# Kernel optimization log

Hardware: AMD Instinct MI355X
Metric: run time of the kernel (lower is better)

Reference implementation:

```python
import jax, jax.numpy as jnp
import numpy as np

N_NODES = 100000
N_EDGES = 3200000
D_IN = 256
D_HID = 97


def setup_inputs() -> dict:
    key = jax.random.key(0)
    k1, k2, k3, k4, k5, k6 = jax.random.split(key, 6)
    x = jax.random.normal(k1, (N_NODES, D_IN), dtype=jnp.float32)
    edge_index = jax.random.randint(k2, (2, N_EDGES), 0, N_NODES, dtype=jnp.int64)
    # GCNConv weights (stored as [in, out]) and biases
    W1 = jax.random.normal(k3, (D_IN, D_HID), dtype=jnp.float32) / np.sqrt(D_IN)
    b1 = jnp.zeros((D_HID,), dtype=jnp.float32)
    W2 = jax.random.normal(k4, (D_HID, D_HID), dtype=jnp.float32) / np.sqrt(D_HID)
    b2 = jnp.zeros((D_HID,), dtype=jnp.float32)
    return {"x": x, "edge_index": edge_index, "W1": W1, "b1": b1, "W2": W2, "b2": b2}


def reference(x, edge_index, W1, b1, W2, b2):
    # PyG GCNConv: add self-loops, symmetric degree normalization,
    # out[i] = sum_j norm_ij * (x[j] @ W) + b
    N = x.shape[0]
    self_idx = jnp.arange(N, dtype=edge_index.dtype)
    src = jnp.concatenate([edge_index[0], self_idx])  # source j
    dst = jnp.concatenate([edge_index[1], self_idx])  # target i
    deg = jax.ops.segment_sum(jnp.ones_like(dst, dtype=x.dtype), dst, num_segments=N)
    dinv = jnp.where(deg > 0, 1.0 / jnp.sqrt(deg), 0.0)
    norm = dinv[src] * dinv[dst]  # [E+N]

    def gcn(h, W, b):
        h = h @ W  # dense linear transform first (out_dim small)
        msg = h[src] * norm[:, None]  # gather + scale
        agg = jax.ops.segment_sum(msg, dst, num_segments=N)  # scatter-add
        return agg + b

    h = jax.nn.relu(gcn(x, W1, b1))
    out = gcn(h, W2, b2)
    return out
```

## Files before the change

kernel.cpp:

```cpp
#include <hip/hip_runtime.h>
#include <hip/hip_fp16.h>
#include <stdint.h>

#define D_IN 256
#define D_H  97
#define RST  96
#define NPB  512
#define NBMAX 256
#define CHUNK 4096

typedef _Float16 f16;
typedef f16   f16x8 __attribute__((ext_vector_type(8)));
typedef float f32x4 __attribute__((ext_vector_type(4)));

__device__ __forceinline__ int load_idx(const void* p, int is64, long long pos) {
  if (is64) return (int)(((const long long*)p)[pos]);
  return ((const int*)p)[pos];
}

__global__ void detect_kernel(const void* ei, long long E, int* flag) {
  const int* p32 = (const int*)ei;
  long long stride = E / 1024; if (stride < 1) stride = 1;
  int tid = threadIdx.x;
  int bad = 0;
  for (int s = 0; s < 4; ++s) {
    long long k = ((long long)tid * 4 + s) * stride;
    if (k < E) {
      if (p32[2 * k + 1] != 0) bad = 1;
    }
  }
  __shared__ int sh_bad;
  if (tid == 0) sh_bad = 0;
  __syncthreads();
  if (bad) atomicOr(&sh_bad, 1);
  __syncthreads();
  if (tid == 0) *flag = sh_bad ? 0 : 1;
}

__global__ __launch_bounds__(256) void bucket_scatter_direct(
    const void* ei, const int* __restrict__ flag, int* __restrict__ bcur,
    unsigned int* __restrict__ bsd, long long E, int nbuck, int cap) {
  __shared__ unsigned int packs[CHUNK];
  __shared__ unsigned char bkts[CHUNK];
  __shared__ int hist[NBMAX];
  __shared__ int gpos[NBMAX];
  __shared__ int cur[NBMAX];
  int tid = threadIdx.x;
  if (tid < NBMAX) { hist[tid] = 0; cur[tid] = 0; }
  __syncthreads();
  int f = *flag;
  long long base = (long long)blockIdx.x * CHUNK;
  int cnt = (int)((E - base < CHUNK) ? (E - base) : CHUNK);
  #pragma unroll 4
  for (int i = tid; i < cnt; i += 256) {
    long long e = base + i;
    int s = load_idx(ei, f, e);
    int d = load_idx(ei, f, E + e);
    int b = d >> 9;
    packs[i] = ((unsigned int)(d & (NPB - 1)) << 17) | (unsigned int)s;
    bkts[i] = (unsigned char)b;
    atomicAdd(&hist[b], 1);
  }
  __syncthreads();
  if (tid < nbuck) { int h = hist[tid]; if (h) gpos[tid] = atomicAdd(&bcur[tid], h); }
  __syncthreads();
  #pragma unroll 4
  for (int i = tid; i < cnt; i += 256) {
    int b = bkts[i];
    int r = atomicAdd(&cur[b], 1);
    int idx = gpos[b] + r;
    if (idx < cap) bsd[(size_t)b * cap + idx] = packs[i];
  }
}

__global__ void bucket_scan2(const int* __restrict__ bcur, int* __restrict__ bstart,
                             int* __restrict__ row_start, int N, int nbuck, int cap) {
  __shared__ int sh[256];
  int tid = threadIdx.x;
  int v = (tid < nbuck) ? min(bcur[tid], cap) : 0;
  sh[tid] = v;
  __syncthreads();
  for (int off = 1; off < 256; off <<= 1) {
    int a = (tid >= off) ? sh[tid - off] : 0;
    __syncthreads();
    sh[tid] += a;
    __syncthreads();
  }
  if (tid < nbuck) bstart[tid] = sh[tid] - v;
  if (tid == 255) { bstart[nbuck] = sh[255]; row_start[N] = sh[255]; }
}

__global__ __launch_bounds__(256) void bucket_finalize(
    const unsigned int* __restrict__ bsd, const int* __restrict__ bcur,
    const int* __restrict__ bstart,
    int* __restrict__ row_start, float* __restrict__ dinv,
    int* __restrict__ csr_src, int N, int cap) {
  __shared__ int h[NPB];
  __shared__ int rs[NPB];
  __shared__ int cur[NPB];
  __shared__ int wsum[4];
  int b = blockIdx.x, tid = threadIdx.x;
  int lane = tid & 63, wid = tid >> 6;
  h[2 * tid] = 0; h[2 * tid + 1] = 0;
  cur[2 * tid] = 0; cur[2 * tid + 1] = 0;
  __syncthreads();
  int d0 = b * cap;
  int cnt = min(bcur[b], cap);
  for (int i = tid; i < cnt; i += 256) atomicAdd(&h[bsd[d0 + i] >> 17], 1);
  __syncthreads();
  int a0 = h[2 * tid], a1 = h[2 * tid + 1];
  int tsum = a0 + a1;
  int incl = tsum;
  #pragma unroll
  for (int off = 1; off < 64; off <<= 1) {
    int n = __shfl_up(incl, off, 64);
    if (lane >= off) incl += n;
  }
  if (lane == 63) wsum[wid] = incl;
  __syncthreads();
  int woff = 0;
  for (int k = 0; k < wid; ++k) woff += wsum[k];
  int excl = woff + incl - tsum + bstart[b];
  rs[2 * tid] = excl;
  rs[2 * tid + 1] = excl + a0;
  int node0 = b * NPB;
  int n0 = node0 + 2 * tid, n1 = node0 + 2 * tid + 1;
  if (n0 < N) { row_start[n0] = excl;      dinv[n0] = rsqrtf((float)(a0 + 1)); }
  if (n1 < N) { row_start[n1] = excl + a0; dinv[n1] = rsqrtf((float)(a1 + 1)); }
  __syncthreads();
  for (int i = tid; i < cnt; i += 256) {
    unsigned int p = bsd[d0 + i];
    int r = p >> 17;
    int s = (int)(p & 0x1FFFFu);
    int rel = atomicAdd(&cur[r], 1);
    csr_src[rs[r] + rel] = s;
  }
}

__global__ void prep_kernel(const float* __restrict__ W1, const float* __restrict__ b1,
                            const float* __restrict__ W2, const float* __restrict__ b2,
                            f16* __restrict__ W1lin, f16* __restrict__ W2lin,
                            float* __restrict__ b1p, float* __restrict__ b2p) {
  int idx = blockIdx.x * blockDim.x + threadIdx.x;
  const int n1 = 8 * 7 * 512;
  const int n2 = 4 * 7 * 512;
  if (idx < n1) {
    int fid = idx >> 3, hh = idx & 7;
    int lane = fid & 63, fg = fid >> 6;
    int kb = fg / 7, cg = fg % 7;
    int c = cg * 16 + (lane & 15);
    int k = kb * 32 + (lane >> 4) * 8 + hh;
    W1lin[idx] = (f16)((c < D_H && k < 256) ? W1[k * D_H + c] : 0.f);
  } else if (idx < n1 + n2) {
    int j = idx - n1;
    int fid = j >> 3, hh = j & 7;
    int lane = fid & 63, fg = fid >> 6;
    int kb = fg / 7, cg = fg % 7;
    int c = cg * 16 + (lane & 15);
    int k = kb * 32 + (lane >> 4) * 8 + hh;
    W2lin[j] = (f16)((c < D_H && k < D_H) ? W2[k * D_H + c] : 0.f);
  } else if (idx < n1 + n2 + 128) {
    int c = idx - (n1 + n2);
    b1p[c] = (c < D_H) ? b1[c] : 0.0f;
  } else if (idx < n1 + n2 + 256) {
    int c = idx - (n1 + n2 + 128);
    b2p[c] = (c < D_H) ? b2[c] : 0.0f;
  }
}

template<int KI, bool IN_HALF>
__global__ __launch_bounds__(256) void mfma_gemm(
    const float* __restrict__ Af, const f16* __restrict__ Ah,
    const __half2* __restrict__ sideA,
    const f16* __restrict__ Wlin, const float* __restrict__ dinv,
    f16* __restrict__ C, __half2* __restrict__ sideC, int N) {
  int tid = threadIdx.x, wave = tid >> 6, lane = tid & 63;
  int row0 = blockIdx.x * 128;
  int m = lane & 15, q = lane >> 4;
  int kf = q * 8;
  int r0 = row0 + wave * 32 + m;
  int r1 = r0 + 16;
  int rr0 = (r0 < N) ? r0 : 0;
  int rr1 = (r1 < N) ? r1 : 0;
  const f16* wbase = Wlin + lane * 8;

  f16x8 a0[KI], a1[KI];
  #pragma unroll
  for (int kb = 0; kb < KI; ++kb) {
    if constexpr (!IN_HALF) {
      const float* p0 = &Af[(size_t)rr0 * 256 + kb * 32 + kf];
      const float* p1 = &Af[(size_t)rr1 * 256 + kb * 32 + kf];
      float4 u0 = *(const float4*)p0, u1 = *(const float4*)(p0 + 4);
      float4 w0 = *(const float4*)p1, w1 = *(const float4*)(p1 + 4);
      f16x8 t0, t1;
      t0[0] = (f16)u0.x; t0[1] = (f16)u0.y; t0[2] = (f16)u0.z; t0[3] = (f16)u0.w;
      t0[4] = (f16)u1.x; t0[5] = (f16)u1.y; t0[6] = (f16)u1.z; t0[7] = (f16)u1.w;
      t1[0] = (f16)w0.x; t1[1] = (f16)w0.y; t1[2] = (f16)w0.z; t1[3] = (f16)w0.w;
      t1[4] = (f16)w1.x; t1[5] = (f16)w1.y; t1[6] = (f16)w1.z; t1[7] = (f16)w1.w;
      a0[kb] = t0; a1[kb] = t1;
    } else {
      if (kb < KI - 1) {
        a0[kb] = *(const f16x8*)&Ah[(size_t)rr0 * RST + kb * 32 + kf];
        a1[kb] = *(const f16x8*)&Ah[(size_t)rr1 * RST + kb * 32 + kf];
      } else {
        f16x8 z0, z1;
        #pragma unroll
        for (int j = 0; j < 8; ++j) { z0[j] = (f16)0.f; z1[j] = (f16)0.f; }
        if (q == 0) {
          z0[0] = ((const f16*)sideA)[2 * rr0];
          z1[0] = ((const f16*)sideA)[2 * rr1];
        }
        a0[kb] = z0; a1[kb] = z1;
      }
    }
  }

  f32x4 acc[2][7];
  #pragma unroll
  for (int mg = 0; mg < 2; ++mg)
    #pragma unroll
    for (int cg = 0; cg < 7; ++cg)
      #pragma unroll
      for (int j = 0; j < 4; ++j) acc[mg][cg][j] = 0.f;

  #pragma unroll
  for (int kb = 0; kb < KI; ++kb) {
    #pragma unroll
    for (int cg = 0; cg < 7; ++cg) {
      f16x8 b = *(const f16x8*)&wbase[(kb * 7 + cg) * 512];
      acc[0][cg] = __builtin_amdgcn_mfma_f32_16x16x32_f16(a0[kb], b, acc[0][cg], 0, 0, 0);
      acc[1][cg] = __builtin_amdgcn_mfma_f32_16x16x32_f16(a1[kb], b, acc[1][cg], 0, 0, 0);
    }
  }

  int colb = m, rq = q * 4;
  #pragma unroll
  for (int mg = 0; mg < 2; ++mg) {
    #pragma unroll
    for (int j = 0; j < 4; ++j) {
      int r = row0 + wave * 32 + mg * 16 + rq + j;
      if (r >= N) continue;
      float dv = dinv[r];
      #pragma unroll
      for (int cg = 0; cg < 7; ++cg) {
        int c = cg * 16 + colb;
        float val = acc[mg][cg][j] * dv;
        if (c < 96)       C[(size_t)r * RST + c] = (f16)val;
        else if (c == 96) sideC[r] = __floats2half2_rn(val, 0.f);
      }
    }
  }
}

template<bool OUT_HALF, bool DO_RELU>
__global__ __launch_bounds__(256) void agg_kernel(
    const __half* __restrict__ t, const __half2* __restrict__ side,
    const int* __restrict__ csr_src, const int* __restrict__ row_start,
    const float* __restrict__ dinv, const float* __restrict__ bias,
    void* __restrict__ outp, __half2* __restrict__ side_out, int node_base, int N) {
  int lane = threadIdx.x & 63;
  int node = node_base + blockIdx.x * (blockDim.x >> 6) + (threadIdx.x >> 6);
  if (node >= N || lane >= 49) return;
  const char* gbase = (lane < 48) ? (const char*)t + lane * 4 : (const char*)side;
  unsigned gscale = (lane < 48) ? (unsigned)(RST * 2) : 4u;
  auto GATHER = [&](int j) -> float2 {
    return __half22float2(*(const __half2*)(gbase + (size_t)((unsigned)j * gscale)));
  };
  int s = row_start[node], epd = row_start[node + 1];
  float di = dinv[node];
  float2 v = GATHER(node);
  float ax = v.x, ay = v.y;
  int e = s;
  while ((e & 3) && e < epd) {
    float2 u = GATHER(csr_src[e]);
    ax += u.x; ay += u.y; ++e;
  }
  for (; e + 8 <= epd; e += 8) {
    int4 q0 = *(const int4*)(csr_src + e);
    int4 q1 = *(const int4*)(csr_src + e + 4);
    float2 u0 = GATHER(q0.x), u1 = GATHER(q0.y), u2 = GATHER(q0.z), u3 = GATHER(q0.w);
    float2 u4 = GATHER(q1.x), u5 = GATHER(q1.y), u6 = GATHER(q1.z), u7 = GATHER(q1.w);
    ax += ((u0.x + u1.x) + (u2.x + u3.x)) + ((u4.x + u5.x) + (u6.x + u7.x));
    ay += ((u0.y + u1.y) + (u2.y + u3.y)) + ((u4.y + u5.y) + (u6.y + u7.y));
  }
  if (e + 4 <= epd) {
    int4 q0 = *(const int4*)(csr_src + e);
    float2 u0 = GATHER(q0.x), u1 = GATHER(q0.y), u2 = GATHER(q0.z), u3 = GATHER(q0.w);
    ax += (u0.x + u1.x) + (u2.x + u3.x);
    ay += (u0.y + u1.y) + (u2.y + u3.y);
    e += 4;
  }
  for (; e < epd; ++e) {
    float2 u = GATHER(csr_src[e]);
    ax += u.x; ay += u.y;
  }
  int c0 = 2 * lane;
  ax = ax * di + bias[c0];
  ay = ay * di + bias[c0 + 1];
  if (DO_RELU) { ax = fmaxf(ax, 0.f); ay = fmaxf(ay, 0.f); }
  if (OUT_HALF) {
    if (lane < 48) ((__half2*)((__half*)outp + (size_t)node * RST))[lane] = __floats2half2_rn(ax, ay);
    else           side_out[node] = __floats2half2_rn(ax, 0.f);
  } else {
    float* o = (float*)outp + (size_t)node * D_H;
    if (lane < 48) { o[c0] = ax; o[c0 + 1] = ay; }
    else           o[96] = ax;
  }
}

extern "C" void kernel_launch(void* const* d_in, const int* in_sizes, int n_in,
                              void* d_out, int out_size, void* d_ws, size_t ws_size,
                              hipStream_t stream) {
  const float* x  = (const float*)d_in[0];
  const void*  ei = d_in[1];
  const float* W1 = (const float*)d_in[2];
  const float* b1 = (const float*)d_in[3];
  const float* W2 = (const float*)d_in[4];
  const float* b2 = (const float*)d_in[5];
  int N = in_sizes[0] / D_IN;
  long long E = (long long)in_sizes[1] / 2;
  int nbuck = (N + NPB - 1) / NPB;
  int cap = (int)(E / nbuck) + 8192;

  char* base = (char*)d_ws;
  size_t off = 0;
  auto alloc = [&](size_t bytes) -> void* {
    void* p = base + off;
    off = (off + bytes + 255) & ~(size_t)255;
    return p;
  };
  int*    flag      = (int*)alloc(4);
  float*  dinv      = (float*)alloc((size_t)N * 4);
  int*    row_start = (int*)alloc((size_t)(N + 1) * 4);
  int*    bcur      = (int*)alloc((size_t)(nbuck + 1) * 4);
  int*    bstart    = (int*)alloc((size_t)(nbuck + 1) * 4);
  int*    csr_src   = (int*)alloc((size_t)E * 4);
  unsigned int* bsd = (unsigned int*)alloc((size_t)nbuck * cap * 4);
  f16*    W1lin     = (f16*)alloc((size_t)8 * 7 * 512 * 2);
  f16*    W2lin     = (f16*)alloc((size_t)4 * 7 * 512 * 2);
  float*  b1p       = (float*)alloc(128 * 4);
  float*  b2p       = (float*)alloc(128 * 4);
  f16*    t1        = (f16*)alloc((size_t)N * RST * 2 + 256);
  __half2* sideT    = (__half2*)alloc((size_t)N * 4 + 256);
  f16*    h1        = (f16*)alloc((size_t)N * RST * 2 + 256);
  __half2* sideH    = (__half2*)alloc((size_t)N * 4 + 256);

  hipMemsetAsync(bcur, 0, (size_t)(nbuck + 1) * 4, stream);
  detect_kernel<<<1, 256, 0, stream>>>(ei, E, flag);
  bucket_scatter_direct<<<(int)((E + CHUNK - 1) / CHUNK), 256, 0, stream>>>(
      ei, flag, bcur, bsd, E, nbuck, cap);
  bucket_scan2<<<1, 256, 0, stream>>>(bcur, bstart, row_start, N, nbuck, cap);
  bucket_finalize<<<nbuck, 256, 0, stream>>>(bsd, bcur, bstart, row_start, dinv, csr_src, N, cap);
  prep_kernel<<<(8 * 7 * 512 + 4 * 7 * 512 + 256 + 255) / 256, 256, 0, stream>>>(
      W1, b1, W2, b2, W1lin, W2lin, b1p, b2p);

  int gGemm = (N + 127) / 128;
  int half = N / 2;
  int gA0 = (half + 3) / 4;
  int gA1 = (N - half + 3) / 4;

  mfma_gemm<8, false><<<gGemm, 256, 0, stream>>>(
      x, nullptr, nullptr, W1lin, dinv, t1, sideT, N);
  agg_kernel<true, true><<<gA0, 256, 0, stream>>>(
      (const __half*)t1, sideT, csr_src, row_start, dinv, b1p, h1, sideH, 0, N);
  agg_kernel<true, true><<<gA1, 256, 0, stream>>>(
      (const __half*)t1, sideT, csr_src, row_start, dinv, b1p, h1, sideH, half, N);
  mfma_gemm<4, true><<<gGemm, 256, 0, stream>>>(
      nullptr, h1, sideH, W2lin, dinv, t1, sideT, N);
  agg_kernel<false, false><<<gA0, 256, 0, stream>>>(
      (const __half*)t1, sideT, csr_src, row_start, dinv, b2p, d_out, nullptr, 0, N);
  agg_kernel<false, false><<<gA1, 256, 0, stream>>>(
      (const __half*)t1, sideT, csr_src, row_start, dinv, b2p, d_out, nullptr, half, N);
}
```

Baseline: 374.2 us.

## Fuse second-layer GEMM into first aggregation and fold bucket scan into finalize

Layer 1's aggregation now multiplies each node's ReLU output by W2 from shared memory, so the second MFMA GEMM and the h1 round trip through global memory go away. The bucket prefix scan is recomputed inside every bucket_finalize block, and the bcur memset moves into detect_kernel, which removes two launches. The risk is that each 512-thread agg block must first copy the full ~19KB W2 into LDS, and per-node scalar GEMV work is added to a gather-bound kernel. The split agg launches are also merged into one.

New measurement: 396.5 us. 6.0% more time.

```diff
diff --git a/kernel.cpp b/kernel.cpp
--- a/kernel.cpp
+++ b/kernel.cpp
@@ -10,6 +10,7 @@
 #define CHUNK 4096
 
 typedef _Float16 f16;
+typedef f16   f16x2 __attribute__((ext_vector_type(2)));
 typedef f16   f16x8 __attribute__((ext_vector_type(8)));
 typedef float f32x4 __attribute__((ext_vector_type(4)));
 
@@ -18,10 +19,12 @@
   return ((const int*)p)[pos];
 }
 
-__global__ void detect_kernel(const void* ei, long long E, int* flag) {
+__global__ void detect_kernel(const void* ei, long long E, int* flag,
+                              int* __restrict__ bcur, int nbuck) {
   const int* p32 = (const int*)ei;
   long long stride = E / 1024; if (stride < 1) stride = 1;
   int tid = threadIdx.x;
+  for (int i = tid; i <= nbuck; i += 256) bcur[i] = 0;
   int bad = 0;
   for (int s = 0; s < 4; ++s) {
     long long k = ((long long)tid * 4 + s) * stride;
@@ -73,39 +76,32 @@
   }
 }
 
-__global__ void bucket_scan2(const int* __restrict__ bcur, int* __restrict__ bstart,
-                             int* __restrict__ row_start, int N, int nbuck, int cap) {
-  __shared__ int sh[256];
-  int tid = threadIdx.x;
-  int v = (tid < nbuck) ? min(bcur[tid], cap) : 0;
-  sh[tid] = v;
-  __syncthreads();
-  for (int off = 1; off < 256; off <<= 1) {
-    int a = (tid >= off) ? sh[tid - off] : 0;
-    __syncthreads();
-    sh[tid] += a;
-    __syncthreads();
-  }
-  if (tid < nbuck) bstart[tid] = sh[tid] - v;
-  if (tid == 255) { bstart[nbuck] = sh[255]; row_start[N] = sh[255]; }
-}
-
 __global__ __launch_bounds__(256) void bucket_finalize(
     const unsigned int* __restrict__ bsd, const int* __restrict__ bcur,
-    const int* __restrict__ bstart,
     int* __restrict__ row_start, float* __restrict__ dinv,
-    int* __restrict__ csr_src, int N, int cap) {
+    int* __restrict__ csr_src, int N, int cap, int nbuck) {
+  __shared__ int sc[256];
   __shared__ int h[NPB];
   __shared__ int rs[NPB];
   __shared__ int cur[NPB];
   __shared__ int wsum[4];
   int b = blockIdx.x, tid = threadIdx.x;
   int lane = tid & 63, wid = tid >> 6;
+  int v = (tid < nbuck) ? min(bcur[tid], cap) : 0;
+  sc[tid] = v;
   h[2 * tid] = 0; h[2 * tid + 1] = 0;
   cur[2 * tid] = 0; cur[2 * tid + 1] = 0;
   __syncthreads();
+  for (int o = 1; o < 256; o <<= 1) {
+    int a = (tid >= o) ? sc[tid - o] : 0;
+    __syncthreads();
+    sc[tid] += a;
+    __syncthreads();
+  }
+  int cnt = min(bcur[b], cap);
+  int base = sc[b] - cnt;
+  if (b == 0 && tid == 0) row_start[N] = sc[255];
   int d0 = b * cap;
-  int cnt = min(bcur[b], cap);
   for (int i = tid; i < cnt; i += 256) atomicAdd(&h[bsd[d0 + i] >> 17], 1);
   __syncthreads();
   int a0 = h[2 * tid], a1 = h[2 * tid + 1];
@@ -120,7 +116,7 @@
   __syncthreads();
   int woff = 0;
   for (int k = 0; k < wid; ++k) woff += wsum[k];
-  int excl = woff + incl - tsum + bstart[b];
+  int excl = woff + incl - tsum + base;
   rs[2 * tid] = excl;
   rs[2 * tid + 1] = excl + a0;
   int node0 = b * NPB;
@@ -139,11 +135,11 @@
 
 __global__ void prep_kernel(const float* __restrict__ W1, const float* __restrict__ b1,
                             const float* __restrict__ W2, const float* __restrict__ b2,
-                            f16* __restrict__ W1lin, f16* __restrict__ W2lin,
+                            f16* __restrict__ W1lin, f16* __restrict__ W2g,
                             float* __restrict__ b1p, float* __restrict__ b2p) {
   int idx = blockIdx.x * blockDim.x + threadIdx.x;
   const int n1 = 8 * 7 * 512;
-  const int n2 = 4 * 7 * 512;
+  const int n2 = 98 * 98;
   if (idx < n1) {
     int fid = idx >> 3, hh = idx & 7;
     int lane = fid & 63, fg = fid >> 6;
@@ -152,13 +148,8 @@
     int k = kb * 32 + (lane >> 4) * 8 + hh;
     W1lin[idx] = (f16)((c < D_H && k < 256) ? W1[k * D_H + c] : 0.f);
   } else if (idx < n1 + n2) {
-    int j = idx - n1;
-    int fid = j >> 3, hh = j & 7;
-    int lane = fid & 63, fg = fid >> 6;
-    int kb = fg / 7, cg = fg % 7;
-    int c = cg * 16 + (lane & 15);
-    int k = kb * 32 + (lane >> 4) * 8 + hh;
-    W2lin[j] = (f16)((c < D_H && k < D_H) ? W2[k * D_H + c] : 0.f);
+    int j = idx - n1; int k = j / 98, c = j % 98;
+    W2g[j] = (f16)((k < D_H && c < D_H) ? W2[k * D_H + c] : 0.f);
   } else if (idx < n1 + n2 + 128) {
     int c = idx - (n1 + n2);
     b1p[c] = (c < D_H) ? b1[c] : 0.0f;
@@ -168,12 +159,11 @@
   }
 }
 
-template<int KI, bool IN_HALF>
-__global__ __launch_bounds__(256) void mfma_gemm(
-    const float* __restrict__ Af, const f16* __restrict__ Ah,
-    const __half2* __restrict__ sideA,
-    const f16* __restrict__ Wlin, const float* __restrict__ dinv,
+__global__ __launch_bounds__(256) void mfma_gemm1(
+    const float* __restrict__ Af, const f16* __restrict__ Wlin,
+    const float* __restrict__ dinv,
     f16* __restrict__ C, __half2* __restrict__ sideC, int N) {
+  const int KI = 8;
   int tid = threadIdx.x, wave = tid >> 6, lane = tid & 63;
   int row0 = blockIdx.x * 128;
   int m = lane & 15, q = lane >> 4;
@@ -187,32 +177,16 @@
   f16x8 a0[KI], a1[KI];
   #pragma unroll
   for (int kb = 0; kb < KI; ++kb) {
-    if constexpr (!IN_HALF) {
-      const float* p0 = &Af[(size_t)rr0 * 256 + kb * 32 + kf];
-      const float* p1 = &Af[(size_t)rr1 * 256 + kb * 32 + kf];
-      float4 u0 = *(const float4*)p0, u1 = *(const float4*)(p0 + 4);
-      float4 w0 = *(const float4*)p1, w1 = *(const float4*)(p1 + 4);
-      f16x8 t0, t1;
-      t0[0] = (f16)u0.x; t0[1] = (f16)u0.y; t0[2] = (f16)u0.z; t0[3] = (f16)u0.w;
-      t0[4] = (f16)u1.x; t0[5] = (f16)u1.y; t0[6] = (f16)u1.z; t0[7] = (f16)u1.w;
-      t1[0] = (f16)w0.x; t1[1] = (f16)w0.y; t1[2] = (f16)w0.z; t1[3] = (f16)w0.w;
-      t1[4] = (f16)w1.x; t1[5] = (f16)w1.y; t1[6] = (f16)w1.z; t1[7] = (f16)w1.w;
-      a0[kb] = t0; a1[kb] = t1;
-    } else {
-      if (kb < KI - 1) {
-        a0[kb] = *(const f16x8*)&Ah[(size_t)rr0 * RST + kb * 32 + kf];
-        a1[kb] = *(const f16x8*)&Ah[(size_t)rr1 * RST + kb * 32 + kf];
-      } else {
-        f16x8 z0, z1;
-        #pragma unroll
-        for (int j = 0; j < 8; ++j) { z0[j] = (f16)0.f; z1[j] = (f16)0.f; }
-        if (q == 0) {
-          z0[0] = ((const f16*)sideA)[2 * rr0];
-          z1[0] = ((const f16*)sideA)[2 * rr1];
-        }
-        a0[kb] = z0; a1[kb] = z1;
-      }
-    }
+    const float* p0 = &Af[(size_t)rr0 * 256 + kb * 32 + kf];
+    const float* p1 = &Af[(size_t)rr1 * 256 + kb * 32 + kf];
+    float4 u0 = *(const float4*)p0, u1 = *(const float4*)(p0 + 4);
+    float4 w0 = *(const float4*)p1, w1 = *(const float4*)(p1 + 4);
+    f16x8 t0, t1;
+    t0[0] = (f16)u0.x; t0[1] = (f16)u0.y; t0[2] = (f16)u0.z; t0[3] = (f16)u0.w;
+    t0[4] = (f16)u1.x; t0[5] = (f16)u1.y; t0[6] = (f16)u1.z; t0[7] = (f16)u1.w;
+    t1[0] = (f16)w0.x; t1[1] = (f16)w0.y; t1[2] = (f16)w0.z; t1[3] = (f16)w0.w;
+    t1[4] = (f16)w1.x; t1[5] = (f16)w1.y; t1[6] = (f16)w1.z; t1[7] = (f16)w1.w;
+    a0[kb] = t0; a1[kb] = t1;
   }
 
   f32x4 acc[2][7];
@@ -252,25 +226,31 @@
   }
 }
 
-template<bool OUT_HALF, bool DO_RELU>
-__global__ __launch_bounds__(256) void agg_kernel(
+__global__ __launch_bounds__(512) void agg_gemv(
     const __half* __restrict__ t, const __half2* __restrict__ side,
     const int* __restrict__ csr_src, const int* __restrict__ row_start,
-    const float* __restrict__ dinv, const float* __restrict__ bias,
-    void* __restrict__ outp, __half2* __restrict__ side_out, int node_base, int N) {
-  int lane = threadIdx.x & 63;
-  int node = node_base + blockIdx.x * (blockDim.x >> 6) + (threadIdx.x >> 6);
+    const float* __restrict__ dinv, const float* __restrict__ b1p,
+    const f16* __restrict__ W2g,
+    f16* __restrict__ t2, __half2* __restrict__ side2, int N) {
+  __shared__ f16 W2s[98 * 98];
+  __shared__ float hbuf[8][98];
+  int tid = threadIdx.x;
+  for (int i = tid; i < 98 * 98 / 2; i += 512)
+    ((f16x2*)W2s)[i] = ((const f16x2*)W2g)[i];
+  __syncthreads();
+  int wave = tid >> 6, lane = tid & 63;
+  int node = blockIdx.x * 8 + wave;
   if (node >= N || lane >= 49) return;
+
   const char* gbase = (lane < 48) ? (const char*)t + lane * 4 : (const char*)side;
   unsigned gscale = (lane < 48) ? (unsigned)(RST * 2) : 4u;
   auto GATHER = [&](int j) -> float2 {
     return __half22float2(*(const __half2*)(gbase + (size_t)((unsigned)j * gscale)));
   };
-  int s = row_start[node], epd = row_start[node + 1];
+  int e = row_start[node], epd = row_start[node + 1];
   float di = dinv[node];
   float2 v = GATHER(node);
   float ax = v.x, ay = v.y;
-  int e = s;
   while ((e & 3) && e < epd) {
     float2 u = GATHER(csr_src[e]);
     ax += u.x; ay += u.y; ++e;
@@ -295,17 +275,81 @@
     ax += u.x; ay += u.y;
   }
   int c0 = 2 * lane;
+  ax = fmaxf(ax * di + b1p[c0], 0.f);
+  ay = fmaxf(ay * di + b1p[c0 + 1], 0.f);
+  hbuf[wave][c0] = ax;
+  if (c0 + 1 < 98) hbuf[wave][c0 + 1] = ay;
+
+  float s0 = 0.f, s1 = 0.f;
+  const float* hl = hbuf[wave];
+  #pragma unroll 4
+  for (int k = 0; k < 96; k += 2) {
+    float h0 = hl[k], h1 = hl[k + 1];
+    f16x2 w0 = *(const f16x2*)&W2s[k * 98 + c0];
+    f16x2 w1 = *(const f16x2*)&W2s[(k + 1) * 98 + c0];
+    s0 += h0 * (float)w0[0] + h1 * (float)w1[0];
+    s1 += h0 * (float)w0[1] + h1 * (float)w1[1];
+  }
+  {
+    float h96 = hl[96];
+    f16x2 w96 = *(const f16x2*)&W2s[96 * 98 + c0];
+    s0 += h96 * (float)w96[0];
+    s1 += h96 * (float)w96[1];
+  }
+  s0 *= di; s1 *= di;
+  if (lane < 48) {
+    *(__half2*)(&t2[(size_t)node * RST + c0]) = __floats2half2_rn(s0, s1);
+  } else {
+    side2[node] = __floats2half2_rn(s0, 0.f);
+  }
+}
+
+__global__ __launch_bounds__(256) void agg_out(
+    const __half* __restrict__ t, const __half2* __restrict__ side,
+    const int* __restrict__ csr_src, const int* __restrict__ row_start,
+    const float* __restrict__ dinv, const float* __restrict__ bias,
+    float* __restrict__ outp, int N) {
+  int lane = threadIdx.x & 63;
+  int node = blockIdx.x * (blockDim.x >> 6) + (threadIdx.x >> 6);
+  if (node >= N || lane >= 49) return;
+  const char* gbase = (lane < 48) ? (const char*)t + lane * 4 : (const char*)side;
+  unsigned gscale = (lane < 48) ? (unsigned)(RST * 2) : 4u;
+  auto GATHER = [&](int j) -> float2 {
+    return __half22float2(*(const __half2*)(gbase + (size_t)((unsigned)j * gscale)));
+  };
+  int e = row_start[node], epd = row_start[node + 1];
+  float di = dinv[node];
+  float2 v = GATHER(node);
+  float ax = v.x, ay = v.y;
+  while ((e & 3) && e < epd) {
+    float2 u = GATHER(csr_src[e]);
+    ax += u.x; ay += u.y; ++e;
+  }
+  for (; e + 8 <= epd; e += 8) {
+    int4 q0 = *(const int4*)(csr_src + e);
+    int4 q1 = *(const int4*)(csr_src + e + 4);
+    float2 u0 = GATHER(q0.x), u1 = GATHER(q0.y), u2 = GATHER(q0.z), u3 = GATHER(q0.w);
+    float2 u4 = GATHER(q1.x), u5 = GATHER(q1.y), u6 = GATHER(q1.z), u7 = GATHER(q1.w);
+    ax += ((u0.x + u1.x) + (u2.x + u3.x)) + ((u4.x + u5.x) + (u6.x + u7.x));
+    ay += ((u0.y + u1.y) + (u2.y + u3.y)) + ((u4.y + u5.y) + (u6.y + u7.y));
+  }
+  if (e + 4 <= epd) {
+    int4 q0 = *(const int4*)(csr_src + e);
+    float2 u0 = GATHER(q0.x), u1 = GATHER(q0.y), u2 = GATHER(q0.z), u3 = GATHER(q0.w);
+    ax += (u0.x + u1.x) + (u2.x + u3.x);
+    ay += (u0.y + u1.y) + (u2.y + u3.y);
+    e += 4;
+  }
+  for (; e < epd; ++e) {
+    float2 u = GATHER(csr_src[e]);
+    ax += u.x; ay += u.y;
+  }
+  int c0 = 2 * lane;
   ax = ax * di + bias[c0];
   ay = ay * di + bias[c0 + 1];
-  if (DO_RELU) { ax = fmaxf(ax, 0.f); ay = fmaxf(ay, 0.f); }
-  if (OUT_HALF) {
-    if (lane < 48) ((__half2*)((__half*)outp + (size_t)node * RST))[lane] = __floats2half2_rn(ax, ay);
-    else           side_out[node] = __floats2half2_rn(ax, 0.f);
-  } else {
-    float* o = (float*)outp + (size_t)node * D_H;
-    if (lane < 48) { o[c0] = ax; o[c0 + 1] = ay; }
-    else           o[96] = ax;
-  }
+  float* o = outp + (size_t)node * D_H;
+  if (lane < 48) { o[c0] = ax; o[c0 + 1] = ay; }
+  else           o[96] = ax;
 }
 
 extern "C" void kernel_launch(void* const* d_in, const int* in_sizes, int n_in,
@@ -333,42 +377,26 @@
   float*  dinv      = (float*)alloc((size_t)N * 4);
   int*    row_start = (int*)alloc((size_t)(N + 1) * 4);
   int*    bcur      = (int*)alloc((size_t)(nbuck + 1) * 4);
-  int*    bstart    = (int*)alloc((size_t)(nbuck + 1) * 4);
   int*    csr_src   = (int*)alloc((size_t)E * 4);
   unsigned int* bsd = (unsigned int*)alloc((size_t)nbuck * cap * 4);
   f16*    W1lin     = (f16*)alloc((size_t)8 * 7 * 512 * 2);
-  f16*    W2lin     = (f16*)alloc((size_t)4 * 7 * 512 * 2);
+  f16*    W2g       = (f16*)alloc((size_t)98 * 98 * 2);
   float*  b1p       = (float*)alloc(128 * 4);
   float*  b2p       = (float*)alloc(128 * 4);
   f16*    t1        = (f16*)alloc((size_t)N * RST * 2 + 256);
   __half2* sideT    = (__half2*)alloc((size_t)N * 4 + 256);
-  f16*    h1        = (f16*)alloc((size_t)N * RST * 2 + 256);
-  __half2* sideH    = (__half2*)alloc((size_t)N * 4 + 256);
-
-  hipMemsetAsync(bcur, 0, (size_t)(nbuck + 1) * 4, stream);
-  detect_kernel<<<1, 256, 0, stream>>>(ei, E, flag);
+  f16*    t2        = (f16*)alloc((size_t)N * RST * 2 + 256);
+  __half2* sideT2   = (__half2*)alloc((size_t)N * 4 + 256);
+
+  detect_kernel<<<1, 256, 0, stream>>>(ei, E, flag, bcur, nbuck);
   bucket_scatter_direct<<<(int)((E + CHUNK - 1) / CHUNK), 256, 0, stream>>>(
       ei, flag, bcur, bsd, E, nbuck, cap);
-  bucket_scan2<<<1, 256, 0, stream>>>(bcur, bstart, row_start, N, nbuck, cap);
-  bucket_finalize<<<nbuck, 256, 0, stream>>>(bsd, bcur, bstart, row_start, dinv, csr_src, N, cap);
-  prep_kernel<<<(8 * 7 * 512 + 4 * 7 * 512 + 256 + 255) / 256, 256, 0, stream>>>(
-      W1, b1, W2, b2, W1lin, W2lin, b1p, b2p);
-
-  int gGemm = (N + 127) / 128;
-  int half = N / 2;
-  int gA0 = (half + 3) / 4;
-  int gA1 = (N - half + 3) / 4;
-
-  mfma_gemm<8, false><<<gGemm, 256, 0, stream>>>(
-      x, nullptr, nullptr, W1lin, dinv, t1, sideT, N);
-  agg_kernel<true, true><<<gA0, 256, 0, stream>>>(
-      (const __half*)t1, sideT, csr_src, row_start, dinv, b1p, h1, sideH, 0, N);
-  agg_kernel<true, true><<<gA1, 256, 0, stream>>>(
-      (const __half*)t1, sideT, csr_src, row_start, dinv, b1p, h1, sideH, half, N);
-  mfma_gemm<4, true><<<gGemm, 256, 0, stream>>>(
-      nullptr, h1, sideH, W2lin, dinv, t1, sideT, N);
-  agg_kernel<false, false><<<gA0, 256, 0, stream>>>(
-      (const __half*)t1, sideT, csr_src, row_start, dinv, b2p, d_out, nullptr, 0, N);
-  agg_kernel<false, false><<<gA1, 256, 0, stream>>>(
-      (const __half*)t1, sideT, csr_src, row_start, dinv, b2p, d_out, nullptr, half, N);
-}
+  bucket_finalize<<<nbuck, 256, 0, stream>>>(bsd, bcur, row_start, dinv, csr_src, N, cap, nbuck);
+  prep_kernel<<<(8 * 7 * 512 + 98 * 98 + 256 + 255) / 256, 256, 0, stream>>>(
+      W1, b1, W2, b2, W1lin, W2g, b1p, b2p);
+  mfma_gemm1<<<(N + 127) / 128, 256, 0, stream>>>(x, W1lin, dinv, t1, sideT, N);
+  agg_gemv<<<(N + 7) / 8, 512, 0, stream>>>(
+      (const __half*)t1, sideT, csr_src, row_start, dinv, b1p, W2g, t2, sideT2, N);
+  agg_out<<<(N + 3) / 4, 256, 0, stream>>>(
+      (const __half*)t2, sideT2, csr_src, row_start, dinv, b2p, (float*)d_out, N);
+}
```
